# Kernel tuning notes

Hardware: AMD Instinct MI355X
Metric: run time of the kernel (lower is better)

The kernel has to match this reference:

```python
import jax, jax.numpy as jnp
import numpy as np

N_NODES = 100000
N_EDGES = 1600000
N_GRAPHS = 64
D_IN, D_HID, D_OUT = 256, 128, 64
EPS = 1e-5


def gcn_conv(x, edge_index, edge_weight, W, b):
    """PyG GCNConv: add_self_loops=True, normalize=True (sym deg norm), bias."""
    n = x.shape[0]
    row = jnp.concatenate([edge_index[0], jnp.arange(n)])      # source
    col = jnp.concatenate([edge_index[1], jnp.arange(n)])      # target
    w = jnp.concatenate([edge_weight, jnp.ones((n,), x.dtype)])
    deg = jax.ops.segment_sum(w, col, num_segments=n)
    dinv = jnp.where(deg > 0, jax.lax.rsqrt(jnp.maximum(deg, EPS)), 0.0)
    norm = dinv[row] * w * dinv[col]                           # [E+N]
    h = x @ W                                                  # [N, out]
    msg = h[row] * norm[:, None]                               # [E+N, out]
    out = jax.ops.segment_sum(msg, col, num_segments=n)
    return out + b


def layer_norm(x, gamma, beta):
    mu = jnp.mean(x, axis=-1, keepdims=True)
    var = jnp.mean(jnp.square(x - mu), axis=-1, keepdims=True)
    return (x - mu) * jax.lax.rsqrt(var + EPS) * gamma + beta


def setup_inputs() -> dict:
    key = jax.random.key(0)
    ks = jax.random.split(key, 12)
    x = jax.random.normal(ks[0], (N_NODES, D_IN), jnp.float32)
    edge_index = jax.random.randint(ks[1], (2, N_EDGES), 0, N_NODES, jnp.int32)
    edge_weight = jax.random.uniform(ks[2], (N_EDGES,), jnp.float32)
    batch = jnp.sort(jax.random.randint(ks[3], (N_NODES,), 0, N_GRAPHS, jnp.int32))
    s1 = 1.0 / np.sqrt(D_IN)
    s2 = 1.0 / np.sqrt(D_HID)
    return {
        "x": x, "edge_index": edge_index, "edge_weight": edge_weight, "batch": batch,
        "W1": jax.random.uniform(ks[4], (D_IN, D_HID), jnp.float32, -s1, s1),
        "b1": jnp.zeros((D_HID,), jnp.float32),
        "g1": jnp.ones((D_HID,), jnp.float32),
        "bt1": jnp.zeros((D_HID,), jnp.float32),
        "W2": jax.random.uniform(ks[5], (D_HID, D_OUT), jnp.float32, -s2, s2),
        "b2": jnp.zeros((D_OUT,), jnp.float32),
        "g2": jnp.ones((D_OUT,), jnp.float32),
        "bt2": jnp.zeros((D_OUT,), jnp.float32),
    }


def reference(x, edge_index, edge_weight, batch, W1, b1, g1, bt1, W2, b2, g2, bt2):
    # ConvLayer 1: GCNConv -> relu -> LayerNorm(node)
    h = gcn_conv(x, edge_index, edge_weight, W1, b1)
    h = layer_norm(jax.nn.relu(h), g1, bt1)
    # dropout is identity in eval mode
    # ConvLayer 2
    h = gcn_conv(h, edge_index, edge_weight, W2, b2)
    h = layer_norm(jax.nn.relu(h), g2, bt2)
    # global mean pool over batch vector
    sums = jax.ops.segment_sum(h, batch, num_segments=N_GRAPHS)
    cnts = jax.ops.segment_sum(jnp.ones((h.shape[0],), h.dtype), batch, num_segments=N_GRAPHS)
    pooled = sums / jnp.maximum(cnts, 1.0)[:, None]
    return jax.nn.sigmoid(pooled)
```

## Files before the change

kernel.cpp:

```cpp
#include <hip/hip_runtime.h>
#include <cstdint>

#define EPSV 1e-5f

typedef __bf16 bf16x8 __attribute__((ext_vector_type(8)));
typedef __bf16 bf16x2 __attribute__((ext_vector_type(2)));
typedef float  f32x4  __attribute__((ext_vector_type(4)));
typedef unsigned long long u64;

__global__ __launch_bounds__(256) void k_degacc(const int* __restrict__ ei,
                                                const float* __restrict__ ew,
                                                u64* __restrict__ dc,
                                                unsigned short* __restrict__ rank,
                                                int E) {
    const int e = blockIdx.x * 256 + threadIdx.x;
    if (e < E) {
        const int c = ei[E + e];
        const u64 pack = (1ull << 40) | (u64)(ew[e] * 16777216.0f);
        const u64 old = atomicAdd(&dc[c], pack);
        rank[e] = (unsigned short)(old >> 40);
    }
}

__global__ __launch_bounds__(256) void k_scanA(const u64* __restrict__ dc,
                                               float* __restrict__ dinv,
                                               int* __restrict__ cnt,
                                               int* __restrict__ bsum, int N) {
    __shared__ int ws[4];
    const int i = blockIdx.x * 256 + threadIdx.x;
    int v = 0;
    if (i < N) {
        const u64 p = dc[i];
        v = (int)(p >> 40);
        const float deg = 1.0f + (float)(p & 0xFFFFFFFFFFull) * (1.0f / 16777216.0f);
        dinv[i] = rsqrtf(deg);
        cnt[i] = v;
    }
#pragma unroll
    for (int o = 32; o >= 1; o >>= 1) v += __shfl_xor(v, o);
    if ((threadIdx.x & 63) == 0) ws[threadIdx.x >> 6] = v;
    __syncthreads();
    if (threadIdx.x == 0) bsum[blockIdx.x] = ws[0] + ws[1] + ws[2] + ws[3];
}

__global__ __launch_bounds__(256) void k_scan2(int* __restrict__ bsum, int NB) {
    __shared__ int carry;
    __shared__ int wsum[4];
    if (threadIdx.x == 0) carry = 0;
    __syncthreads();
    const int lane = threadIdx.x & 63, w = threadIdx.x >> 6;
    for (int base = 0; base < NB; base += 256) {
        const int i = base + threadIdx.x;
        const int v = (i < NB) ? bsum[i] : 0;
        int s = v;
#pragma unroll
        for (int o = 1; o < 64; o <<= 1) {
            const int t = __shfl_up(s, o);
            if (lane >= o) s += t;
        }
        if (lane == 63) wsum[w] = s;
        __syncthreads();
        int add = carry;
        for (int k = 0; k < w; ++k) add += wsum[k];
        const int tot = wsum[0] + wsum[1] + wsum[2] + wsum[3];
        if (i < NB) bsum[i] = add + s - v;
        __syncthreads();
        if (threadIdx.x == 0) carry += tot;
        __syncthreads();
    }
}

__global__ __launch_bounds__(256) void k_scan3(const int* __restrict__ cnt,
                                               const int* __restrict__ bsum,
                                               int* __restrict__ off, int N) {
    __shared__ int wsum[4];
    const int i = blockIdx.x * 256 + threadIdx.x;
    const int v = (i < N) ? cnt[i] : 0;
    const int lane = threadIdx.x & 63, w = threadIdx.x >> 6;
    int s = v;
#pragma unroll
    for (int o = 1; o < 64; o <<= 1) {
        const int t = __shfl_up(s, o);
        if (lane >= o) s += t;
    }
    if (lane == 63) wsum[w] = s;
    __syncthreads();
    int add = bsum[blockIdx.x];
    for (int k = 0; k < w; ++k) add += wsum[k];
    if (i < N) off[i] = add + s - v;
}

__global__ __launch_bounds__(256) void k_fill(const int* __restrict__ ei,
                                              const float* __restrict__ ew,
                                              const float* __restrict__ dinv,
                                              const int* __restrict__ off,
                                              const unsigned short* __restrict__ rank,
                                              float2* __restrict__ ern, int E) {
    const int e = blockIdx.x * 256 + threadIdx.x;
    if (e >= E) return;
    const int r = ei[e];
    const int c = ei[E + e];
    const int p = off[c] + (int)rank[e];
    ern[p] = make_float2(__int_as_float(r), dinv[r] * ew[e] * dinv[c]);
}

__global__ __launch_bounds__(256) void k_wcvt(const float* __restrict__ W1,
                                              __bf16* __restrict__ Wt1,
                                              const float* __restrict__ W2,
                                              __bf16* __restrict__ Wt2) {
    const int idx = blockIdx.x * 256 + threadIdx.x;
    if (idx < 256 * 128) {
        const int k = idx >> 7, c = idx & 127;
        Wt1[(((k >> 3) << 7) + c) * 8 + (k & 7)] = (__bf16)W1[idx];
    } else if (idx < 256 * 128 + 128 * 64) {
        const int j = idx - 256 * 128;
        const int k = j >> 6, c = j & 63;
        Wt2[(((k >> 3) << 6) + c) * 8 + (k & 7)] = (__bf16)W2[j];
    }
}

template <int K, int NOUT, bool ABF16>
__global__ __launch_bounds__(256) void k_mm(const void* __restrict__ Xv,
                                            const __bf16* __restrict__ WtB,
                                            __bf16* __restrict__ H, int N) {
    constexpr int NCB = NOUT / 16;
    constexpr int NKB = K / 32;
    const int tid = threadIdx.x;
    const int w = tid >> 6, l = tid & 63;
    const int r0 = l & 15, kq = l >> 4;
    const long tb0 = (long)blockIdx.x * 128 + w * 32;
    const long ar0 = (tb0 + r0) < N ? (tb0 + r0) : (long)N - 1;
    const long ar1 = (tb0 + 16 + r0) < N ? (tb0 + 16 + r0) : (long)N - 1;

    f32x4 acc[2][NCB];
#pragma unroll
    for (int rf = 0; rf < 2; ++rf)
#pragma unroll
        for (int cb = 0; cb < NCB; ++cb) acc[rf][cb] = (f32x4){0.f, 0.f, 0.f, 0.f};

#define LDA(kb, a0, a1)                                                          \
    {                                                                            \
        const int koff = (kb) * 32 + kq * 8;                                     \
        if constexpr (ABF16) {                                                   \
            a0 = *reinterpret_cast<const bf16x8*>((const __bf16*)Xv + ar0 * K + koff); \
            a1 = *reinterpret_cast<const bf16x8*>((const __bf16*)Xv + ar1 * K + koff); \
        } else {                                                                 \
            const float* p0 = (const float*)Xv + ar0 * K + koff;                 \
            const float* p1 = (const float*)Xv + ar1 * K + koff;                 \
            const float4 u0 = *reinterpret_cast<const float4*>(p0);              \
            const float4 u1 = *reinterpret_cast<const float4*>(p0 + 4);          \
            const float4 u2 = *reinterpret_cast<const float4*>(p1);              \
            const float4 u3 = *reinterpret_cast<const float4*>(p1 + 4);          \
            a0[0] = (__bf16)u0.x; a0[1] = (__bf16)u0.y; a0[2] = (__bf16)u0.z;    \
            a0[3] = (__bf16)u0.w; a0[4] = (__bf16)u1.x; a0[5] = (__bf16)u1.y;    \
            a0[6] = (__bf16)u1.z; a0[7] = (__bf16)u1.w;                          \
            a1[0] = (__bf16)u2.x; a1[1] = (__bf16)u2.y; a1[2] = (__bf16)u2.z;    \
            a1[3] = (__bf16)u2.w; a1[4] = (__bf16)u3.x; a1[5] = (__bf16)u3.y;    \
            a1[6] = (__bf16)u3.z; a1[7] = (__bf16)u3.w;                          \
        }                                                                        \
    }

#define LDB(kb, b)                                                               \
    {                                                                            \
        const __bf16* bp = WtB + (long)(((kb) * 4 + kq) * NOUT + r0) * 8;        \
        _Pragma("unroll") for (int cb = 0; cb < NCB; ++cb)                       \
            b[cb] = *reinterpret_cast<const bf16x8*>(bp + cb * 128);             \
    }

    bf16x8 aC0, aC1, aN0, aN1;
    bf16x8 bC[NCB], bN[NCB];
    LDA(0, aC0, aC1);
    LDB(0, bC);
#pragma unroll
    for (int kb = 0; kb < NKB; ++kb) {
        if (kb + 1 < NKB) {
            LDA(kb + 1, aN0, aN1);
            LDB(kb + 1, bN);
        }
#pragma unroll
        for (int cb = 0; cb < NCB; ++cb) {
            acc[0][cb] = __builtin_amdgcn_mfma_f32_16x16x32_bf16(aC0, bC[cb], acc[0][cb], 0, 0, 0);
            acc[1][cb] = __builtin_amdgcn_mfma_f32_16x16x32_bf16(aC1, bC[cb], acc[1][cb], 0, 0, 0);
        }
        aC0 = aN0; aC1 = aN1;
#pragma unroll
        for (int cb = 0; cb < NCB; ++cb) bC[cb] = bN[cb];
    }
#undef LDA
#undef LDB

    const int orow = kq * 4;
#pragma unroll
    for (int rf = 0; rf < 2; ++rf)
#pragma unroll
        for (int cb = 0; cb < NCB; ++cb)
#pragma unroll
            for (int r = 0; r < 4; ++r) {
                const long gr = tb0 + rf * 16 + orow + r;
                if (gr < N) H[gr * NOUT + cb * 16 + r0] = (__bf16)acc[rf][cb][r];
            }
}

__global__ __launch_bounds__(256) void k_gat128(const __bf16* __restrict__ H,
                                                const int* __restrict__ off,
                                                const int* __restrict__ cnt,
                                                const float2* __restrict__ ern,
                                                const float* __restrict__ dinv,
                                                const float* __restrict__ bias,
                                                const float* __restrict__ gm,
                                                const float* __restrict__ bt,
                                                __bf16* __restrict__ Out, int N) {
    const long wv = ((long)blockIdx.x * 256 + threadIdx.x) >> 6;
    const int lane = threadIdx.x & 63;
    if (wv >= N) return;
    const int s = off[wv];
    const int n = cnt[wv];
    const float d = dinv[wv];
    const bf16x2* Hp = reinterpret_cast<const bf16x2*>(H);

    const bf16x2 h0 = Hp[wv * 64 + lane];
    float ax = (float)h0[0] * d * d, ay = (float)h0[1] * d * d;

    int e = 0;
    for (; e + 8 <= n; e += 8) {
        float2 q[8];
#pragma unroll
        for (int j = 0; j < 8; ++j) q[j] = ern[s + e + j];
        bf16x2 v[8];
#pragma unroll
        for (int j = 0; j < 8; ++j)
            v[j] = Hp[(long)__float_as_int(q[j].x) * 64 + lane];
#pragma unroll
        for (int j = 0; j < 8; ++j) {
            ax = fmaf(q[j].y, (float)v[j][0], ax);
            ay = fmaf(q[j].y, (float)v[j][1], ay);
        }
    }
    for (; e < n; ++e) {
        const float2 q = ern[s + e];
        const bf16x2 v = Hp[(long)__float_as_int(q.x) * 64 + lane];
        ax = fmaf(q.y, (float)v[0], ax);
        ay = fmaf(q.y, (float)v[1], ay);
    }

    const float ux = fmaxf(ax + bias[2 * lane], 0.f);
    const float uy = fmaxf(ay + bias[2 * lane + 1], 0.f);
    float s1 = ux + uy, s2 = ux * ux + uy * uy;
#pragma unroll
    for (int o = 32; o >= 1; o >>= 1) {
        s1 += __shfl_xor(s1, o);
        s2 += __shfl_xor(s2, o);
    }
    const float mu = s1 * (1.f / 128.f);
    const float var = s2 * (1.f / 128.f) - mu * mu;
    const float rs = rsqrtf(var + EPSV);
    bf16x2 ob;
    ob[0] = (__bf16)((ux - mu) * rs * gm[2 * lane] + bt[2 * lane]);
    ob[1] = (__bf16)((uy - mu) * rs * gm[2 * lane + 1] + bt[2 * lane + 1]);
    reinterpret_cast<bf16x2*>(Out)[wv * 64 + lane] = ob;
}

__global__ __launch_bounds__(256) void k_gat64(const __bf16* __restrict__ H,
                                               const int* __restrict__ off,
                                               const int* __restrict__ cnt,
                                               const float2* __restrict__ ern,
                                               const float* __restrict__ dinv,
                                               const float* __restrict__ bias,
                                               const float* __restrict__ gm,
                                               const float* __restrict__ bt,
                                               float* __restrict__ Out, int N) {
    const long wv = ((long)blockIdx.x * 256 + threadIdx.x) >> 6;
    const int lane = threadIdx.x & 63;
    if (wv >= N) return;
    const int s = off[wv];
    const int n = cnt[wv];
    const float d = dinv[wv];

    float acc = (float)H[wv * 64 + lane] * d * d;
    int e = 0;
    for (; e + 8 <= n; e += 8) {
        float2 q[8];
#pragma unroll
        for (int j = 0; j < 8; ++j) q[j] = ern[s + e + j];
        float v[8];
#pragma unroll
        for (int j = 0; j < 8; ++j)
            v[j] = (float)H[(long)__float_as_int(q[j].x) * 64 + lane];
#pragma unroll
        for (int j = 0; j < 8; ++j) acc = fmaf(q[j].y, v[j], acc);
    }
    for (; e < n; ++e) {
        const float2 q = ern[s + e];
        acc = fmaf(q.y, (float)H[(long)__float_as_int(q.x) * 64 + lane], acc);
    }

    const float u = fmaxf(acc + bias[lane], 0.f);
    float s1 = u, s2 = u * u;
#pragma unroll
    for (int o = 32; o >= 1; o >>= 1) {
        s1 += __shfl_xor(s1, o);
        s2 += __shfl_xor(s2, o);
    }
    const float mu = s1 * (1.f / 64.f);
    const float var = s2 * (1.f / 64.f) - mu * mu;
    const float rs = rsqrtf(var + EPSV);
    Out[wv * 64 + lane] = (u - mu) * rs * gm[lane] + bt[lane];
}

__global__ __launch_bounds__(256) void k_pool(const float* __restrict__ C,
                                              const int* __restrict__ batch,
                                              float* __restrict__ pool,
                                              int N, int chunk) {
    const int wg = blockIdx.x * 4 + (threadIdx.x >> 6);
    const int lane = threadIdx.x & 63;
    long i = (long)wg * chunk;
    const long end = (i + chunk < (long)N) ? i + chunk : (long)N;
    if (i >= end) return;

    int cur = batch[i];
    float acc = 0.f;
    int cn = 0;
    while (i < end) {
        if (i + 8 <= end && batch[i + 7] == cur) {
            float v[8];
#pragma unroll
            for (int j = 0; j < 8; ++j) v[j] = C[(i + j) * 64 + lane];
            acc += ((v[0] + v[1]) + (v[2] + v[3])) + ((v[4] + v[5]) + (v[6] + v[7]));
            cn += 8;
            i += 8;
            continue;
        }
        const int b = batch[i];
        if (b != cur) {
            unsafeAtomicAdd(&pool[cur * 64 + lane], acc);
            if (lane == 0) unsafeAtomicAdd(&pool[64 * 64 + cur], (float)cn);
            cur = b;
            acc = 0.f;
            cn = 0;
        }
        acc += C[i * 64 + lane];
        ++cn;
        ++i;
    }
    unsafeAtomicAdd(&pool[cur * 64 + lane], acc);
    if (lane == 0) unsafeAtomicAdd(&pool[64 * 64 + cur], (float)cn);
}

__global__ __launch_bounds__(256) void k_final(const float* __restrict__ pool,
                                               float* __restrict__ out) {
    const int i = blockIdx.x * 256 + threadIdx.x;
    if (i < 4096) {
        const int g = i >> 6;
        const float cnt = fmaxf(pool[64 * 64 + g], 1.0f);
        const float v = pool[i] / cnt;
        out[i] = 1.f / (1.f + expf(-v));
    }
}

extern "C" void kernel_launch(void* const* d_in, const int* in_sizes, int n_in,
                              void* d_out, int out_size, void* d_ws, size_t ws_size,
                              hipStream_t stream) {
    const float* x   = (const float*)d_in[0];
    const int*   ei  = (const int*)d_in[1];
    const float* ew  = (const float*)d_in[2];
    const int*   bat = (const int*)d_in[3];
    const float* W1  = (const float*)d_in[4];
    const float* b1  = (const float*)d_in[5];
    const float* g1  = (const float*)d_in[6];
    const float* bt1 = (const float*)d_in[7];
    const float* W2  = (const float*)d_in[8];
    const float* b2  = (const float*)d_in[9];
    const float* g2  = (const float*)d_in[10];
    const float* bt2 = (const float*)d_in[11];
    const int N = in_sizes[3];
    const int E = in_sizes[2];
    const int NB = (N + 255) / 256;

    u64*    dc   = (u64*)d_ws;
    float*  pool = (float*)(dc + N);
    float2* ern  = (float2*)(pool + 64 * 64 + 64);
    __bf16* Ah   = (__bf16*)(ern + E);
    __bf16* Bh   = Ah + (long)N * 128;
    float*  Cf   = (float*)(Bh + (long)N * 128);
    float*  dinv = Cf + (long)N * 64;
    int*    cnt  = (int*)(dinv + N);
    int*    off  = cnt + N;
    int*    bsum = off + N;
    unsigned short* rank = (unsigned short*)(bsum + ((NB + 3) & ~3));
    __bf16* Wt1  = (__bf16*)(rank + E);
    __bf16* Wt2  = Wt1 + 128 * 256;

    const int nbE = (E + 255) / 256;
    const int nbW = (int)(((long)N * 64 + 255) / 256);

    hipMemsetAsync(dc, 0, (size_t)N * 8 + (64 * 64 + 64) * 4, stream);
    k_degacc<<<nbE, 256, 0, stream>>>(ei, ew, dc, rank, E);
    k_scanA<<<NB, 256, 0, stream>>>(dc, dinv, cnt, bsum, N);
    k_scan2<<<1, 256, 0, stream>>>(bsum, NB);
    k_scan3<<<NB, 256, 0, stream>>>(cnt, bsum, off, N);
    k_fill<<<nbE, 256, 0, stream>>>(ei, ew, dinv, off, rank, ern, E);
    k_wcvt<<<(256 * 128 + 128 * 64 + 255) / 256, 256, 0, stream>>>(W1, Wt1, W2, Wt2);

    k_mm<256, 128, false><<<(N + 127) / 128, 256, 0, stream>>>(x, Wt1, Ah, N);
    k_gat128<<<nbW, 256, 0, stream>>>(Ah, off, cnt, ern, dinv, b1, g1, bt1, Bh, N);

    k_mm<128, 64, true><<<(N + 127) / 128, 256, 0, stream>>>(Bh, Wt2, Ah, N);
    k_gat64<<<nbW, 256, 0, stream>>>(Ah, off, cnt, ern, dinv, b2, g2, bt2, Cf, N);

    const int chunk = (N + 1023) / 1024;
    k_pool<<<256, 256, 0, stream>>>(Cf, bat, pool, N, chunk);
    k_final<<<16, 256, 0, stream>>>(pool, (float*)d_out);
}
```

Measured before the change: 337.1 us.

## Store GEMM outputs as FP8 and fuse first GEMM with degree accumulation

The H matrices written by both GEMMs and read by the gather kernels are now stored as FP8 (e4m3 via cvt_pk_fp8) instead of bf16, halving the bytes moved by the random-access neighbour gathers. The first GEMM and the degree/rank atomic accumulation are merged into one launch with disjoint block ranges so they run concurrently, and the weight conversion is moved ahead of it. The cost is a large precision loss in the messages, which risks exceeding tolerance, plus per-element conversion instructions in the gather loops.

```diff
diff --git a/kernel.cpp b/kernel.cpp
--- a/kernel.cpp
+++ b/kernel.cpp
@@ -8,18 +8,9 @@
 typedef float  f32x4  __attribute__((ext_vector_type(4)));
 typedef unsigned long long u64;
 
-__global__ __launch_bounds__(256) void k_degacc(const int* __restrict__ ei,
-                                                const float* __restrict__ ew,
-                                                u64* __restrict__ dc,
-                                                unsigned short* __restrict__ rank,
-                                                int E) {
-    const int e = blockIdx.x * 256 + threadIdx.x;
-    if (e < E) {
-        const int c = ei[E + e];
-        const u64 pack = (1ull << 40) | (u64)(ew[e] * 16777216.0f);
-        const u64 old = atomicAdd(&dc[c], pack);
-        rank[e] = (unsigned short)(old >> 40);
-    }
+__device__ __forceinline__ unsigned char f32_to_fp8(float x) {
+    const int p = __builtin_amdgcn_cvt_pk_fp8_f32(x, x, 0, false);
+    return (unsigned char)(p & 0xFF);
 }
 
 __global__ __launch_bounds__(256) void k_scanA(const u64* __restrict__ dc,
@@ -120,15 +111,14 @@
 }
 
 template <int K, int NOUT, bool ABF16>
-__global__ __launch_bounds__(256) void k_mm(const void* __restrict__ Xv,
-                                            const __bf16* __restrict__ WtB,
-                                            __bf16* __restrict__ H, int N) {
+__device__ __forceinline__ void mm_body(int bid, int tid, const void* __restrict__ Xv,
+                                        const __bf16* __restrict__ WtB,
+                                        unsigned char* __restrict__ H, int N) {
     constexpr int NCB = NOUT / 16;
     constexpr int NKB = K / 32;
-    const int tid = threadIdx.x;
     const int w = tid >> 6, l = tid & 63;
     const int r0 = l & 15, kq = l >> 4;
-    const long tb0 = (long)blockIdx.x * 128 + w * 32;
+    const long tb0 = (long)bid * 128 + w * 32;
     const long ar0 = (tb0 + r0) < N ? (tb0 + r0) : (long)N - 1;
     const long ar1 = (tb0 + 16 + r0) < N ? (tb0 + 16 + r0) : (long)N - 1;
 
@@ -197,11 +187,37 @@
 #pragma unroll
             for (int r = 0; r < 4; ++r) {
                 const long gr = tb0 + rf * 16 + orow + r;
-                if (gr < N) H[gr * NOUT + cb * 16 + r0] = (__bf16)acc[rf][cb][r];
+                if (gr < N) H[gr * NOUT + cb * 16 + r0] = f32_to_fp8(acc[rf][cb][r]);
             }
 }
 
-__global__ __launch_bounds__(256) void k_gat128(const __bf16* __restrict__ H,
+__global__ __launch_bounds__(256) void k_pre(const float* __restrict__ X,
+                                             const __bf16* __restrict__ Wt1,
+                                             unsigned char* __restrict__ H1, int N, int NBM,
+                                             const int* __restrict__ ei,
+                                             const float* __restrict__ ew,
+                                             u64* __restrict__ dc,
+                                             unsigned short* __restrict__ rank, int E) {
+    if ((int)blockIdx.x < NBM) {
+        mm_body<256, 128, false>(blockIdx.x, threadIdx.x, X, Wt1, H1, N);
+    } else {
+        const int e = ((int)blockIdx.x - NBM) * 256 + threadIdx.x;
+        if (e < E) {
+            const int c = ei[E + e];
+            const u64 pack = (1ull << 40) | (u64)(ew[e] * 16777216.0f);
+            const u64 old = atomicAdd(&dc[c], pack);
+            rank[e] = (unsigned short)(old >> 40);
+        }
+    }
+}
+
+__global__ __launch_bounds__(256) void k_mm2(const __bf16* __restrict__ X,
+                                             const __bf16* __restrict__ Wt2,
+                                             unsigned char* __restrict__ H, int N) {
+    mm_body<128, 64, true>(blockIdx.x, threadIdx.x, X, Wt2, H, N);
+}
+
+__global__ __launch_bounds__(256) void k_gat128(const unsigned char* __restrict__ H,
                                                 const int* __restrict__ off,
                                                 const int* __restrict__ cnt,
                                                 const float2* __restrict__ ern,
@@ -216,31 +232,32 @@
     const int s = off[wv];
     const int n = cnt[wv];
     const float d = dinv[wv];
-    const bf16x2* Hp = reinterpret_cast<const bf16x2*>(H);
-
-    const bf16x2 h0 = Hp[wv * 64 + lane];
-    float ax = (float)h0[0] * d * d, ay = (float)h0[1] * d * d;
+    const unsigned short* Hp = reinterpret_cast<const unsigned short*>(H);
+
+    const unsigned int h0 = Hp[wv * 64 + lane];
+    float ax = __builtin_amdgcn_cvt_f32_fp8(h0, 0) * d * d;
+    float ay = __builtin_amdgcn_cvt_f32_fp8(h0, 1) * d * d;
 
     int e = 0;
     for (; e + 8 <= n; e += 8) {
         float2 q[8];
 #pragma unroll
         for (int j = 0; j < 8; ++j) q[j] = ern[s + e + j];
-        bf16x2 v[8];
+        unsigned int u[8];
 #pragma unroll
         for (int j = 0; j < 8; ++j)
-            v[j] = Hp[(long)__float_as_int(q[j].x) * 64 + lane];
+            u[j] = Hp[(long)__float_as_int(q[j].x) * 64 + lane];
 #pragma unroll
         for (int j = 0; j < 8; ++j) {
-            ax = fmaf(q[j].y, (float)v[j][0], ax);
-            ay = fmaf(q[j].y, (float)v[j][1], ay);
+            ax = fmaf(q[j].y, __builtin_amdgcn_cvt_f32_fp8(u[j], 0), ax);
+            ay = fmaf(q[j].y, __builtin_amdgcn_cvt_f32_fp8(u[j], 1), ay);
         }
     }
     for (; e < n; ++e) {
         const float2 q = ern[s + e];
-        const bf16x2 v = Hp[(long)__float_as_int(q.x) * 64 + lane];
-        ax = fmaf(q.y, (float)v[0], ax);
-        ay = fmaf(q.y, (float)v[1], ay);
+        const unsigned int u = Hp[(long)__float_as_int(q.x) * 64 + lane];
+        ax = fmaf(q.y, __builtin_amdgcn_cvt_f32_fp8(u, 0), ax);
+        ay = fmaf(q.y, __builtin_amdgcn_cvt_f32_fp8(u, 1), ay);
     }
 
     const float ux = fmaxf(ax + bias[2 * lane], 0.f);
@@ -260,7 +277,7 @@
     reinterpret_cast<bf16x2*>(Out)[wv * 64 + lane] = ob;
 }
 
-__global__ __launch_bounds__(256) void k_gat64(const __bf16* __restrict__ H,
+__global__ __launch_bounds__(256) void k_gat64(const unsigned char* __restrict__ H,
                                                const int* __restrict__ off,
                                                const int* __restrict__ cnt,
                                                const float2* __restrict__ ern,
@@ -276,22 +293,24 @@
     const int n = cnt[wv];
     const float d = dinv[wv];
 
-    float acc = (float)H[wv * 64 + lane] * d * d;
+    float acc = __builtin_amdgcn_cvt_f32_fp8((unsigned int)H[wv * 64 + lane], 0) * d * d;
     int e = 0;
     for (; e + 8 <= n; e += 8) {
         float2 q[8];
 #pragma unroll
         for (int j = 0; j < 8; ++j) q[j] = ern[s + e + j];
-        float v[8];
+        unsigned int u[8];
 #pragma unroll
         for (int j = 0; j < 8; ++j)
-            v[j] = (float)H[(long)__float_as_int(q[j].x) * 64 + lane];
-#pragma unroll
-        for (int j = 0; j < 8; ++j) acc = fmaf(q[j].y, v[j], acc);
+            u[j] = H[(long)__float_as_int(q[j].x) * 64 + lane];
+#pragma unroll
+        for (int j = 0; j < 8; ++j)
+            acc = fmaf(q[j].y, __builtin_amdgcn_cvt_f32_fp8(u[j], 0), acc);
     }
     for (; e < n; ++e) {
         const float2 q = ern[s + e];
-        acc = fmaf(q.y, (float)H[(long)__float_as_int(q.x) * 64 + lane], acc);
+        const unsigned int u = H[(long)__float_as_int(q.x) * 64 + lane];
+        acc = fmaf(q.y, __builtin_amdgcn_cvt_f32_fp8(u, 0), acc);
     }
 
     const float u = fmaxf(acc + bias[lane], 0.f);
@@ -379,8 +398,8 @@
     u64*    dc   = (u64*)d_ws;
     float*  pool = (float*)(dc + N);
     float2* ern  = (float2*)(pool + 64 * 64 + 64);
-    __bf16* Ah   = (__bf16*)(ern + E);
-    __bf16* Bh   = Ah + (long)N * 128;
+    unsigned char* Ah = (unsigned char*)(ern + E);
+    __bf16* Bh   = (__bf16*)(Ah + (long)N * 128);
     float*  Cf   = (float*)(Bh + (long)N * 128);
     float*  dinv = Cf + (long)N * 64;
     int*    cnt  = (int*)(dinv + N);
@@ -392,19 +411,21 @@
 
     const int nbE = (E + 255) / 256;
     const int nbW = (int)(((long)N * 64 + 255) / 256);
+    const int NBM = (N + 127) / 128;
 
     hipMemsetAsync(dc, 0, (size_t)N * 8 + (64 * 64 + 64) * 4, stream);
-    k_degacc<<<nbE, 256, 0, stream>>>(ei, ew, dc, rank, E);
+    k_wcvt<<<(256 * 128 + 128 * 64 + 255) / 256, 256, 0, stream>>>(W1, Wt1, W2, Wt2);
+
+    k_pre<<<NBM + nbE, 256, 0, stream>>>(x, Wt1, Ah, N, NBM, ei, ew, dc, rank, E);
+
     k_scanA<<<NB, 256, 0, stream>>>(dc, dinv, cnt, bsum, N);
     k_scan2<<<1, 256, 0, stream>>>(bsum, NB);
     k_scan3<<<NB, 256, 0, stream>>>(cnt, bsum, off, N);
     k_fill<<<nbE, 256, 0, stream>>>(ei, ew, dinv, off, rank, ern, E);
-    k_wcvt<<<(256 * 128 + 128 * 64 + 255) / 256, 256, 0, stream>>>(W1, Wt1, W2, Wt2);
-
-    k_mm<256, 128, false><<<(N + 127) / 128, 256, 0, stream>>>(x, Wt1, Ah, N);
+
     k_gat128<<<nbW, 256, 0, stream>>>(Ah, off, cnt, ern, dinv, b1, g1, bt1, Bh, N);
 
-    k_mm<128, 64, true><<<(N + 127) / 128, 256, 0, stream>>>(Bh, Wt2, Ah, N);
+    k_mm2<<<NBM, 256, 0, stream>>>(Bh, Wt2, Ah, N);
     k_gat64<<<nbW, 256, 0, stream>>>(Ah, off, cnt, ern, dinv, b2, g2, bt2, Cf, N);
 
     const int chunk = (N + 1023) / 1024;
```

Measured after the change: 317.9 us. 1.06x faster.
